# Kernel optimization log

Hardware: AMD Instinct MI355X
Metric: run time of the kernel (lower is better)

The kernel has to match this reference:

```python
import jax, jax.numpy as jnp
import numpy as np

B, T, C, H = 2, 2048, 1024, 16
HD = C // H  # 64

def setup_inputs() -> dict:
    key = jax.random.key(0)
    ks = jax.random.split(key, 9)
    s = 0.02
    return {
        "x": jax.random.normal(ks[0], (B, T, C), jnp.float32),
        "Wq": jax.random.normal(ks[1], (C, C), jnp.float32) * s,
        "bq": jax.random.normal(ks[2], (C,), jnp.float32) * s,
        "Wk": jax.random.normal(ks[3], (C, C), jnp.float32) * s,
        "bk": jax.random.normal(ks[4], (C,), jnp.float32) * s,
        "Wv": jax.random.normal(ks[5], (C, C), jnp.float32) * s,
        "bv": jax.random.normal(ks[6], (C,), jnp.float32) * s,
        "Wp": jax.random.normal(ks[7], (C, C), jnp.float32) * s,
        "bp": jax.random.normal(ks[8], (C,), jnp.float32) * s,
    }

def reference(x, Wq, bq, Wk, bk, Wv, bv, Wp, bp):
    Bb, Tt, Cc = x.shape
    hd = Cc // H
    # project and split heads: [B, H, T, hd]
    def heads(W, b):
        return (x @ W.T + b).reshape(Bb, Tt, H, hd).transpose(0, 2, 1, 3)
    q, k, v = heads(Wq, bq), heads(Wk, bk), heads(Wv, bv)
    scale = 1.0 / np.sqrt(hd).astype(np.float32)
    att = jnp.einsum('bhqd,bhkd->bhqk', q, k) * scale
    causal = jnp.tril(jnp.ones((Tt, Tt), bool))
    att = jnp.where(causal[None, None], att, -jnp.inf)
    att = jax.nn.softmax(att, axis=-1)
    y = jnp.einsum('bhqk,bhkd->bhqd', att, v)
    y = y.transpose(0, 2, 1, 3).reshape(Bb, Tt, Cc)
    return y @ Wp.T + bp
```

## Files before the change

kernel.cpp:

```cpp
#include <hip/hip_runtime.h>
#include <hip/hip_bf16.h>

#define Tsz 2048
#define Csz 1024
#define Hn 16

typedef short s8v __attribute__((ext_vector_type(8)));
typedef short s4v __attribute__((ext_vector_type(4)));
typedef float f4v __attribute__((ext_vector_type(4)));

#define QSCALE (0.125f * 1.44269504088896f)

__device__ __forceinline__ short bf_bits(float x) {
    __hip_bfloat16 t = __float2bfloat16(x);
    return *reinterpret_cast<short*>(&t);
}

__device__ __forceinline__ void gload_lds(const void* g, void* l) {
    __builtin_amdgcn_global_load_lds(
        (const __attribute__((address_space(1))) void*)g,
        (__attribute__((address_space(3))) void*)l, 16, 0, 0);
}

__global__ void cvt6(const float* __restrict__ x, const float* __restrict__ wq,
                     const float* __restrict__ wk, const float* __restrict__ wv,
                     const float* __restrict__ wp,
                     short* __restrict__ xo, short* __restrict__ qo,
                     short* __restrict__ ko, short* __restrict__ vo,
                     short* __restrict__ po) {
    const int bx = blockIdx.x;
    const float* in; short* out; int ib;
    if (bx < 4096) { in = x; out = xo; ib = bx; }
    else {
        const int r = bx - 4096, w = r >> 10;
        ib = r & 1023;
        switch (w) {
            case 0: in = wq; out = qo; break;
            case 1: in = wk; out = ko; break;
            case 2: in = wv; out = vo; break;
            default: in = wp; out = po; break;
        }
    }
    const int i = ib * 1024 + threadIdx.x * 4;
    float4 v = *(const float4*)(in + i);
    short4 o;
    o.x = bf_bits(v.x); o.y = bf_bits(v.y); o.z = bf_bits(v.z); o.w = bf_bits(v.w);
    *(short4*)(out + i) = o;
}

__global__ __launch_bounds__(256, 3) void qkv_gemm(
    const short* __restrict__ X,
    const short* __restrict__ Wq, const short* __restrict__ Wk, const short* __restrict__ Wv,
    const float* __restrict__ bq, const float* __restrict__ bk, const float* __restrict__ bv,
    short* __restrict__ Qo, short* __restrict__ Ko, short* __restrict__ Vto)
{
    const int z = blockIdx.z;
    const short* W = (z == 0) ? Wq : (z == 1) ? Wk : Wv;
    const float* bias = (z == 0) ? bq : (z == 1) ? bk : bv;

    __shared__ __align__(16) short Ash[128 * 32];
    __shared__ __align__(16) short Bsh[128 * 32];
    __shared__ __align__(16) short TR[64 * 72];

    const int tid = threadIdx.x, lane = tid & 63, wave = tid >> 6;
    const int ln = lane & 15, hi = lane >> 4;
    const int m0 = blockIdx.x * 128, n0 = blockIdx.y * 128;
    const int wm = (wave >> 1) * 64, wn = (wave & 1) * 64;

    const short* Ag = X + (size_t)(m0 + (tid >> 2)) * Csz + (tid & 3) * 8;
    const short* Bg = W + (size_t)(n0 + (tid >> 2)) * Csz + (tid & 3) * 8;

    f4v acc[4][4];
    #pragma unroll
    for (int mt = 0; mt < 4; mt++)
        #pragma unroll
        for (int nt = 0; nt < 4; nt++)
            #pragma unroll
            for (int i = 0; i < 4; i++) acc[mt][nt][i] = 0.f;

    for (int k0 = 0; k0 < Csz; k0 += 32) {
        __syncthreads();
        gload_lds(Ag + k0, Ash + tid * 8);
        gload_lds(Ag + k0 + (size_t)64 * Csz, Ash + 2048 + tid * 8);
        gload_lds(Bg + k0, Bsh + tid * 8);
        gload_lds(Bg + k0 + (size_t)64 * Csz, Bsh + 2048 + tid * 8);
        __syncthreads();

        s8v af[4], bfr[4];
        #pragma unroll
        for (int mt = 0; mt < 4; mt++)
            af[mt] = *(const s8v*)(Ash + (wm + mt * 16 + ln) * 32 + hi * 8);
        #pragma unroll
        for (int nt = 0; nt < 4; nt++)
            bfr[nt] = *(const s8v*)(Bsh + (wn + nt * 16 + ln) * 32 + hi * 8);
        #pragma unroll
        for (int mt = 0; mt < 4; mt++)
            #pragma unroll
            for (int nt = 0; nt < 4; nt++)
                acc[mt][nt] = __builtin_amdgcn_mfma_f32_16x16x32_bf16(af[mt], bfr[nt], acc[mt][nt], 0, 0, 0);
    }

    if (z == 2) {
        const int b = m0 >> 11, t0 = m0 & 2047;
        float bvv[4];
        #pragma unroll
        for (int nt = 0; nt < 4; nt++) bvv[nt] = bias[n0 + wn + nt * 16 + ln];
        #pragma unroll
        for (int ph = 0; ph < 4; ph++) {
            const int mh = ph >> 1, nh = ph & 1;
            __syncthreads();
            if ((wave >> 1) == mh && (wave & 1) == nh) {
                #pragma unroll
                for (int mt = 0; mt < 4; mt++)
                    #pragma unroll
                    for (int nt = 0; nt < 4; nt++) {
                        s4v pk;
                        #pragma unroll
                        for (int i = 0; i < 4; i++) pk[i] = bf_bits(acc[mt][nt][i] + bvv[nt]);
                        *(s4v*)(TR + (nt * 16 + ln) * 72 + mt * 16 + hi * 4) = pk;
                    }
            }
            __syncthreads();
            const int chl = tid >> 2, seg = tid & 3;
            const s8v r0 = *(const s8v*)(TR + chl * 72 + seg * 16);
            const s8v r1 = *(const s8v*)(TR + chl * 72 + seg * 16 + 8);
            short* dst = Vto + (size_t)(b * 1024 + n0 + nh * 64 + chl) * Tsz + t0 + mh * 64 + seg * 16;
            *(s8v*)(dst) = r0;
            *(s8v*)(dst + 8) = r1;
        }
        return;
    }

    const float scale = (z == 0) ? QSCALE : 1.0f;
    short* out = (z == 0) ? Qo : Ko;

    #pragma unroll
    for (int nt = 0; nt < 4; nt++) {
        const int col = n0 + wn + nt * 16 + ln;
        const float bvv = bias[col];
        #pragma unroll
        for (int mt = 0; mt < 4; mt++) {
            const int row0 = m0 + wm + mt * 16 + hi * 4;
            #pragma unroll
            for (int i = 0; i < 4; i++)
                out[(size_t)(row0 + i) * Csz + col] = bf_bits((acc[mt][nt][i] + bvv) * scale);
        }
    }
}

__global__ __launch_bounds__(256, 2) void proj_gemm(
    const short* __restrict__ A, const short* __restrict__ W,
    const float* __restrict__ bias, float* __restrict__ out)
{
    __shared__ __align__(16) short Ash[128 * 32];
    __shared__ __align__(16) short Bsh[128 * 32];

    const int tid = threadIdx.x, lane = tid & 63, wave = tid >> 6;
    const int ln = lane & 15, hi = lane >> 4;
    const int m0 = blockIdx.x * 128, n0 = blockIdx.y * 128;
    const int wm = (wave >> 1) * 64, wn = (wave & 1) * 64;

    const short* Ag = A + (size_t)(m0 + (tid >> 2)) * Csz + (tid & 3) * 8;
    const short* Bg = W + (size_t)(n0 + (tid >> 2)) * Csz + (tid & 3) * 8;

    f4v acc[4][4];
    #pragma unroll
    for (int mt = 0; mt < 4; mt++)
        #pragma unroll
        for (int nt = 0; nt < 4; nt++)
            #pragma unroll
            for (int i = 0; i < 4; i++) acc[mt][nt][i] = 0.f;

    for (int k0 = 0; k0 < Csz; k0 += 32) {
        __syncthreads();
        gload_lds(Ag + k0, Ash + tid * 8);
        gload_lds(Ag + k0 + (size_t)64 * Csz, Ash + 2048 + tid * 8);
        gload_lds(Bg + k0, Bsh + tid * 8);
        gload_lds(Bg + k0 + (size_t)64 * Csz, Bsh + 2048 + tid * 8);
        __syncthreads();

        s8v af[4], bfr[4];
        #pragma unroll
        for (int mt = 0; mt < 4; mt++)
            af[mt] = *(const s8v*)(Ash + (wm + mt * 16 + ln) * 32 + hi * 8);
        #pragma unroll
        for (int nt = 0; nt < 4; nt++)
            bfr[nt] = *(const s8v*)(Bsh + (wn + nt * 16 + ln) * 32 + hi * 8);
        #pragma unroll
        for (int mt = 0; mt < 4; mt++)
            #pragma unroll
            for (int nt = 0; nt < 4; nt++)
                acc[mt][nt] = __builtin_amdgcn_mfma_f32_16x16x32_bf16(af[mt], bfr[nt], acc[mt][nt], 0, 0, 0);
    }

    #pragma unroll
    for (int nt = 0; nt < 4; nt++) {
        const int col = n0 + wn + nt * 16 + ln;
        const float bvv = bias[col];
        #pragma unroll
        for (int mt = 0; mt < 4; mt++)
            #pragma unroll
            for (int i = 0; i < 4; i++)
                out[(size_t)(m0 + wm + mt * 16 + hi * 4 + i) * Csz + col] = acc[mt][nt][i] + bvv;
    }
}

__global__ __launch_bounds__(512, 2) void attn7(
    const short* __restrict__ Q, const short* __restrict__ Kg,
    const short* __restrict__ Vt, short* __restrict__ Y)
{
    __shared__ __align__(16) short Ksh[2][64 * 72];
    __shared__ __align__(16) short Vsh[2][64 * 72];
    __shared__ __align__(16) short Psh[8][16 * 72];

    const int tid = threadIdx.x, lane = tid & 63, wave = tid >> 6;
    const int wv = wave & 3, g = wave >> 2;
    const int ln = lane & 15, hi = lane >> 4;
    const int p = blockIdx.x;
    const int qts[2] = { g ? 15 - p : p, g ? 16 + p : 31 - p };
    const int bh = blockIdx.y;
    const size_t base = (size_t)(bh >> 4) * Tsz * Csz + (size_t)(bh & 15) * 64;
    const size_t vtbase = (size_t)bh * 64 * Tsz;
    const int qrel = wv * 16 + ln;
    short* Pq = Psh[wave];

    s8v qf[2][2];
    #pragma unroll
    for (int t = 0; t < 2; t++)
        #pragma unroll
        for (int kk = 0; kk < 2; kk++)
            qf[t][kk] = *(const s8v*)(Q + base + (size_t)(qts[t] * 64 + qrel) * Csz + kk * 32 + hi * 8);

    f4v o[2][4];
    float lsum[2] = {0.f, 0.f};
    #pragma unroll
    for (int t = 0; t < 2; t++)
        #pragma unroll
        for (int dt = 0; dt < 4; dt++)
            #pragma unroll
            for (int i = 0; i < 4; i++) o[t][dt][i] = 0.f;

    const int sr = tid >> 3, sc = (tid & 7) * 8;
    const short* Kp = Kg + base + (size_t)sr * Csz + sc;
    const short* Vp = Vt + vtbase + (size_t)sr * Tsz + sc;
    const int swo = sr * 72 + sc;

    const int nkb = 32 - p;

    s8v kR = *(const s8v*)(Kp);
    s8v vR = *(const s8v*)(Vp);
    *(s8v*)(&Ksh[0][swo]) = kR;
    *(s8v*)(&Vsh[0][swo]) = vR;
    kR = *(const s8v*)(Kp + (size_t)64 * Csz);
    vR = *(const s8v*)(Vp + 64);
    __syncthreads();

    for (int kb = 0; kb < nkb; kb++) {
        const int buf = kb & 1;
        if (kb + 1 < nkb) {
            *(s8v*)(&Ksh[buf ^ 1][swo]) = kR;
            *(s8v*)(&Vsh[buf ^ 1][swo]) = vR;
            const int knx = (kb + 2 < nkb) ? (kb + 2) * 64 : (nkb - 1) * 64;
            kR = *(const s8v*)(Kp + (size_t)knx * Csz);
            vR = *(const s8v*)(Vp + knx);
        }

        s8v kf[2][4], vf[2][4];
        #pragma unroll
        for (int nt = 0; nt < 4; nt++)
            #pragma unroll
            for (int kk = 0; kk < 2; kk++) {
                kf[kk][nt] = *(const s8v*)(&Ksh[buf][(nt * 16 + ln) * 72 + kk * 32 + hi * 8]);
                vf[kk][nt] = *(const s8v*)(&Vsh[buf][(nt * 16 + ln) * 72 + kk * 32 + hi * 8]);
            }

        #pragma unroll
        for (int t = 0; t < 2; t++) {
            if (kb > qts[t]) continue;
            const bool dg = (kb == qts[t]);

            f4v s[4];
            #pragma unroll
            for (int nt = 0; nt < 4; nt++) {
                #pragma unroll
                for (int i = 0; i < 4; i++) s[nt][i] = 0.f;
                s[nt] = __builtin_amdgcn_mfma_f32_16x16x32_bf16(kf[0][nt], qf[t][0], s[nt], 0, 0, 0);
                s[nt] = __builtin_amdgcn_mfma_f32_16x16x32_bf16(kf[1][nt], qf[t][1], s[nt], 0, 0, 0);
            }

            #pragma unroll
            for (int nt = 0; nt < 4; nt++) {
                float pv[4];
                #pragma unroll
                for (int i = 0; i < 4; i++) pv[i] = exp2f(s[nt][i]);
                if (dg) {
                    const int kr = nt * 16 + hi * 4;
                    #pragma unroll
                    for (int i = 0; i < 4; i++)
                        if (kr + i > qrel) pv[i] = 0.f;
                }
                lsum[t] += (pv[0] + pv[1]) + (pv[2] + pv[3]);
                s4v w;
                #pragma unroll
                for (int i = 0; i < 4; i++) w[i] = bf_bits(pv[i]);
                *(s4v*)(Pq + ln * 72 + nt * 16 + hi * 4) = w;
            }
            const s8v pb0 = *(const s8v*)(Pq + ln * 72 + hi * 8);
            const s8v pb1 = *(const s8v*)(Pq + ln * 72 + 32 + hi * 8);

            #pragma unroll
            for (int dt = 0; dt < 4; dt++) {
                o[t][dt] = __builtin_amdgcn_mfma_f32_16x16x32_bf16(vf[0][dt], pb0, o[t][dt], 0, 0, 0);
                o[t][dt] = __builtin_amdgcn_mfma_f32_16x16x32_bf16(vf[1][dt], pb1, o[t][dt], 0, 0, 0);
            }
        }
        __syncthreads();
    }

    #pragma unroll
    for (int t = 0; t < 2; t++) {
        float l = lsum[t];
        l += __shfl_xor(l, 16);
        l += __shfl_xor(l, 32);
        const float inv = 1.0f / l;
        const int qrow = qts[t] * 64 + qrel;
        #pragma unroll
        for (int dt = 0; dt < 4; dt++) {
            s4v w;
            #pragma unroll
            for (int i = 0; i < 4; i++) w[i] = bf_bits(o[t][dt][i] * inv);
            *(s4v*)(Y + base + (size_t)qrow * Csz + dt * 16 + hi * 4) = w;
        }
    }
}

extern "C" void kernel_launch(void* const* d_in, const int* in_sizes, int n_in,
                              void* d_out, int out_size, void* d_ws, size_t ws_size,
                              hipStream_t stream) {
    const float* x  = (const float*)d_in[0];
    const float* Wq = (const float*)d_in[1];
    const float* bq = (const float*)d_in[2];
    const float* Wk = (const float*)d_in[3];
    const float* bk = (const float*)d_in[4];
    const float* Wv = (const float*)d_in[5];
    const float* bv = (const float*)d_in[6];
    const float* Wp = (const float*)d_in[7];
    const float* bp = (const float*)d_in[8];

    char* ws = (char*)d_ws;
    short* Xb  = (short*)(ws);
    short* Wqb = (short*)(ws + (8u  << 20));
    short* Wkb = (short*)(ws + (10u << 20));
    short* Wvb = (short*)(ws + (12u << 20));
    short* Wpb = (short*)(ws + (14u << 20));
    short* Qb  = (short*)(ws + (16u << 20));
    short* Kb  = (short*)(ws + (24u << 20));
    short* Vtb = (short*)(ws + (32u << 20));
    short* Yb  = (short*)(ws + (40u << 20));

    hipLaunchKernelGGL(cvt6, dim3(8192), dim3(256), 0, stream,
                       x, Wq, Wk, Wv, Wp, Xb, Wqb, Wkb, Wvb, Wpb);

    hipLaunchKernelGGL(qkv_gemm, dim3(32, 8, 3), dim3(256), 0, stream,
                       Xb, Wqb, Wkb, Wvb, bq, bk, bv, Qb, Kb, Vtb);

    hipLaunchKernelGGL(attn7, dim3(8, 32), dim3(512), 0, stream, Qb, Kb, Vtb, Yb);

    hipLaunchKernelGGL(proj_gemm, dim3(32, 8), dim3(256), 0, stream, Yb, Wpb, bp, (float*)d_out);
}
```

Before: 191.4 us.

## Use bit-trick bf16 rounding with paired packing and halve proj GEMM N-tile

Replaces the library float-to-bf16 conversion with a simple add-0x8000-and-shift rounding that packs two values per 32-bit word. This applies to the input cast, the QKV epilogue, the attention P tile and the attention output. The projection GEMM tile shrinks from 128x128 to 128x64 and its grid doubles, which gives 512 blocks on the device instead of 256 for better occupancy. The new rounding drops NaN handling and is round-half-up rather than round-to-nearest-even, so results can differ slightly.

```diff
diff --git a/kernel.cpp b/kernel.cpp
--- a/kernel.cpp
+++ b/kernel.cpp
@@ -11,9 +11,13 @@
 
 #define QSCALE (0.125f * 1.44269504088896f)
 
-__device__ __forceinline__ short bf_bits(float x) {
-    __hip_bfloat16 t = __float2bfloat16(x);
-    return *reinterpret_cast<short*>(&t);
+__device__ __forceinline__ unsigned short bfr(float x) {
+    return (unsigned short)((__builtin_bit_cast(unsigned, x) + 0x8000u) >> 16);
+}
+__device__ __forceinline__ unsigned pack2_rn(float a, float b) {
+    const unsigned ua = __builtin_bit_cast(unsigned, a) + 0x8000u;
+    const unsigned ub = __builtin_bit_cast(unsigned, b) + 0x8000u;
+    return (ua >> 16) | (ub & 0xFFFF0000u);
 }
 
 __device__ __forceinline__ void gload_lds(const void* g, void* l) {
@@ -43,9 +47,10 @@
     }
     const int i = ib * 1024 + threadIdx.x * 4;
     float4 v = *(const float4*)(in + i);
-    short4 o;
-    o.x = bf_bits(v.x); o.y = bf_bits(v.y); o.z = bf_bits(v.z); o.w = bf_bits(v.w);
-    *(short4*)(out + i) = o;
+    int2 o;
+    o.x = (int)pack2_rn(v.x, v.y);
+    o.y = (int)pack2_rn(v.z, v.w);
+    *(int2*)(out + i) = o;
 }
 
 __global__ __launch_bounds__(256, 3) void qkv_gemm(
@@ -86,18 +91,18 @@
         gload_lds(Bg + k0 + (size_t)64 * Csz, Bsh + 2048 + tid * 8);
         __syncthreads();
 
-        s8v af[4], bfr[4];
+        s8v af[4], bfr_[4];
         #pragma unroll
         for (int mt = 0; mt < 4; mt++)
             af[mt] = *(const s8v*)(Ash + (wm + mt * 16 + ln) * 32 + hi * 8);
         #pragma unroll
         for (int nt = 0; nt < 4; nt++)
-            bfr[nt] = *(const s8v*)(Bsh + (wn + nt * 16 + ln) * 32 + hi * 8);
+            bfr_[nt] = *(const s8v*)(Bsh + (wn + nt * 16 + ln) * 32 + hi * 8);
         #pragma unroll
         for (int mt = 0; mt < 4; mt++)
             #pragma unroll
             for (int nt = 0; nt < 4; nt++)
-                acc[mt][nt] = __builtin_amdgcn_mfma_f32_16x16x32_bf16(af[mt], bfr[nt], acc[mt][nt], 0, 0, 0);
+                acc[mt][nt] = __builtin_amdgcn_mfma_f32_16x16x32_bf16(af[mt], bfr_[nt], acc[mt][nt], 0, 0, 0);
     }
 
     if (z == 2) {
@@ -114,10 +119,10 @@
                 for (int mt = 0; mt < 4; mt++)
                     #pragma unroll
                     for (int nt = 0; nt < 4; nt++) {
-                        s4v pk;
-                        #pragma unroll
-                        for (int i = 0; i < 4; i++) pk[i] = bf_bits(acc[mt][nt][i] + bvv[nt]);
-                        *(s4v*)(TR + (nt * 16 + ln) * 72 + mt * 16 + hi * 4) = pk;
+                        int2 pk;
+                        pk.x = (int)pack2_rn(acc[mt][nt][0] + bvv[nt], acc[mt][nt][1] + bvv[nt]);
+                        pk.y = (int)pack2_rn(acc[mt][nt][2] + bvv[nt], acc[mt][nt][3] + bvv[nt]);
+                        *(int2*)(TR + (nt * 16 + ln) * 72 + mt * 16 + hi * 4) = pk;
                     }
             }
             __syncthreads();
@@ -143,7 +148,7 @@
             const int row0 = m0 + wm + mt * 16 + hi * 4;
             #pragma unroll
             for (int i = 0; i < 4; i++)
-                out[(size_t)(row0 + i) * Csz + col] = bf_bits((acc[mt][nt][i] + bvv) * scale);
+                out[(size_t)(row0 + i) * Csz + col] = (short)bfr((acc[mt][nt][i] + bvv) * scale);
         }
     }
 }
@@ -153,21 +158,21 @@
     const float* __restrict__ bias, float* __restrict__ out)
 {
     __shared__ __align__(16) short Ash[128 * 32];
-    __shared__ __align__(16) short Bsh[128 * 32];
+    __shared__ __align__(16) short Bsh[64 * 32];
 
     const int tid = threadIdx.x, lane = tid & 63, wave = tid >> 6;
     const int ln = lane & 15, hi = lane >> 4;
-    const int m0 = blockIdx.x * 128, n0 = blockIdx.y * 128;
-    const int wm = (wave >> 1) * 64, wn = (wave & 1) * 64;
+    const int m0 = blockIdx.x * 128, n0 = blockIdx.y * 64;
+    const int wm = (wave >> 1) * 64, wn = (wave & 1) * 32;
 
     const short* Ag = A + (size_t)(m0 + (tid >> 2)) * Csz + (tid & 3) * 8;
     const short* Bg = W + (size_t)(n0 + (tid >> 2)) * Csz + (tid & 3) * 8;
 
-    f4v acc[4][4];
+    f4v acc[4][2];
     #pragma unroll
     for (int mt = 0; mt < 4; mt++)
         #pragma unroll
-        for (int nt = 0; nt < 4; nt++)
+        for (int nt = 0; nt < 2; nt++)
             #pragma unroll
             for (int i = 0; i < 4; i++) acc[mt][nt][i] = 0.f;
 
@@ -176,25 +181,24 @@
         gload_lds(Ag + k0, Ash + tid * 8);
         gload_lds(Ag + k0 + (size_t)64 * Csz, Ash + 2048 + tid * 8);
         gload_lds(Bg + k0, Bsh + tid * 8);
-        gload_lds(Bg + k0 + (size_t)64 * Csz, Bsh + 2048 + tid * 8);
-        __syncthreads();
-
-        s8v af[4], bfr[4];
+        __syncthreads();
+
+        s8v af[4], bfr_[2];
         #pragma unroll
         for (int mt = 0; mt < 4; mt++)
             af[mt] = *(const s8v*)(Ash + (wm + mt * 16 + ln) * 32 + hi * 8);
         #pragma unroll
-        for (int nt = 0; nt < 4; nt++)
-            bfr[nt] = *(const s8v*)(Bsh + (wn + nt * 16 + ln) * 32 + hi * 8);
-        #pragma unroll
-        for (int mt = 0; mt < 4; mt++)
-            #pragma unroll
-            for (int nt = 0; nt < 4; nt++)
-                acc[mt][nt] = __builtin_amdgcn_mfma_f32_16x16x32_bf16(af[mt], bfr[nt], acc[mt][nt], 0, 0, 0);
-    }
-
-    #pragma unroll
-    for (int nt = 0; nt < 4; nt++) {
+        for (int nt = 0; nt < 2; nt++)
+            bfr_[nt] = *(const s8v*)(Bsh + (wn + nt * 16 + ln) * 32 + hi * 8);
+        #pragma unroll
+        for (int mt = 0; mt < 4; mt++)
+            #pragma unroll
+            for (int nt = 0; nt < 2; nt++)
+                acc[mt][nt] = __builtin_amdgcn_mfma_f32_16x16x32_bf16(af[mt], bfr_[nt], acc[mt][nt], 0, 0, 0);
+    }
+
+    #pragma unroll
+    for (int nt = 0; nt < 2; nt++) {
         const int col = n0 + wn + nt * 16 + ln;
         const float bvv = bias[col];
         #pragma unroll
@@ -205,7 +209,7 @@
     }
 }
 
-__global__ __launch_bounds__(512, 2) void attn7(
+__global__ __launch_bounds__(512, 2) void attn9(
     const short* __restrict__ Q, const short* __restrict__ Kg,
     const short* __restrict__ Vt, short* __restrict__ Y)
 {
@@ -300,10 +304,10 @@
                         if (kr + i > qrel) pv[i] = 0.f;
                 }
                 lsum[t] += (pv[0] + pv[1]) + (pv[2] + pv[3]);
-                s4v w;
-                #pragma unroll
-                for (int i = 0; i < 4; i++) w[i] = bf_bits(pv[i]);
-                *(s4v*)(Pq + ln * 72 + nt * 16 + hi * 4) = w;
+                int2 w;
+                w.x = (int)pack2_rn(pv[0], pv[1]);
+                w.y = (int)pack2_rn(pv[2], pv[3]);
+                *(int2*)(Pq + ln * 72 + nt * 16 + hi * 4) = w;
             }
             const s8v pb0 = *(const s8v*)(Pq + ln * 72 + hi * 8);
             const s8v pb1 = *(const s8v*)(Pq + ln * 72 + 32 + hi * 8);
@@ -326,10 +330,10 @@
         const int qrow = qts[t] * 64 + qrel;
         #pragma unroll
         for (int dt = 0; dt < 4; dt++) {
-            s4v w;
-            #pragma unroll
-            for (int i = 0; i < 4; i++) w[i] = bf_bits(o[t][dt][i] * inv);
-            *(s4v*)(Y + base + (size_t)qrow * Csz + dt * 16 + hi * 4) = w;
+            int2 w;
+            w.x = (int)pack2_rn(o[t][dt][0] * inv, o[t][dt][1] * inv);
+            w.y = (int)pack2_rn(o[t][dt][2] * inv, o[t][dt][3] * inv);
+            *(int2*)(Y + base + (size_t)qrow * Csz + dt * 16 + hi * 4) = w;
         }
     }
 }
@@ -364,7 +368,7 @@
     hipLaunchKernelGGL(qkv_gemm, dim3(32, 8, 3), dim3(256), 0, stream,
                        Xb, Wqb, Wkb, Wvb, bq, bk, bv, Qb, Kb, Vtb);
 
-    hipLaunchKernelGGL(attn7, dim3(8, 32), dim3(512), 0, stream, Qb, Kb, Vtb, Yb);
-
-    hipLaunchKernelGGL(proj_gemm, dim3(32, 8), dim3(256), 0, stream, Yb, Wpb, bp, (float*)d_out);
-}
+    hipLaunchKernelGGL(attn9, dim3(8, 32), dim3(512), 0, stream, Qb, Kb, Vtb, Yb);
+
+    hipLaunchKernelGGL(proj_gemm, dim3(32, 16), dim3(256), 0, stream, Yb, Wpb, bp, (float*)d_out);
+}
```

New measurement: 189.1 us. About the same (-1.2%).
